# Performance work log

Hardware: AMD Instinct MI355X
Metric: run time of the kernel (lower is better)

Reference implementation:

```python
import jax, jax.numpy as jnp
import numpy as np

D = 256      # d_model
L = 2        # num_layers
N = 10000    # num_nodes
E = 160000   # num_edges (avg degree 16)
EPS = 1e-5


def _ln(h, g, b):
    m = jnp.mean(h, axis=-1, keepdims=True)
    v = jnp.mean(jnp.square(h - m), axis=-1, keepdims=True)
    return (h - m) / jnp.sqrt(v + EPS) * g + b


def _lrelu(h):
    return jnp.where(h > 0, h, 0.2 * h)


def setup_inputs() -> dict:
    key = jax.random.key(0)
    ks = jax.random.split(key, 24)
    p = lambda k, shape: (jax.random.normal(k, shape, dtype=jnp.float32) * 0.05)
    inp = {
        "edge_index": jax.random.randint(ks[0], (2, E), 0, N),
        "x": jax.random.normal(ks[1], (N, D), dtype=jnp.float32),
        # per-layer attention / FF params (torch Linear convention: W is [out, in])
        "Wq": p(ks[2], (L, D, D)), "bq": p(ks[3], (L, D)),
        "Wk": p(ks[4], (L, D, D)), "bk": p(ks[5], (L, D)),
        "Wv": p(ks[6], (L, D, D)), "bv": p(ks[7], (L, D)),
        "Wff": p(ks[8], (L, D, D)), "bff": p(ks[9], (L, D)),
        # LayerNorm params
        "ga": jnp.ones((L, D), jnp.float32), "ba": jnp.zeros((L, D), jnp.float32),
        "gf": jnp.ones((L, D), jnp.float32), "bf": jnp.zeros((L, D), jnp.float32),
        "gfin": jnp.ones((D,), jnp.float32), "bfin": jnp.zeros((D,), jnp.float32),
        # head MLP
        "W3": p(ks[10], (3 * D, D)), "b3": p(ks[11], (3 * D,)),
        "W4": p(ks[12], (3 * D, 3 * D)), "b4": p(ks[13], (3 * D,)),
        "W5": p(ks[14], (D, 3 * D)), "b5": p(ks[15], (D,)),
        "Wvec": p(ks[16], (1, D)), "bvec": p(ks[17], (1,)),
    }
    return inp


def reference(edge_index, x, Wq, bq, Wk, bk, Wv, bv, Wff, bff,
              ga, ba, gf, bf, gfin, bfin, W3, b3, W4, b4, W5, b5, Wvec, bvec):
    num_nodes = x.shape[0]
    src = edge_index[0]  # [E]
    dst = edge_index[1]  # [E] (segment-softmax target)
    x_i = x[src]         # [E, D]
    query = x[dst]       # [E, D] (x_j)
    for i in range(Wq.shape[0]):
        q = query @ Wq[i].T + bq[i]            # [E, D]
        k = x_i @ Wk[i].T + bk[i]
        v = x_i @ Wv[i].T + bv[i]
        alpha = jnp.sum(q * k, axis=-1)        # [E]
        # segment softmax over dst
        amax = jax.ops.segment_max(alpha, dst, num_segments=num_nodes)
        e = jnp.exp(alpha - amax[dst])
        denom = jax.ops.segment_sum(e, dst, num_segments=num_nodes)
        attn = e / denom[dst]                  # [E]
        attn_out = q + attn[:, None] * v       # [E, D]
        query = _ln(attn_out, ga[i], ba[i])
        query = query @ Wff[i].T + bff[i]
    query = _lrelu(query)
    query = _ln(query, gf[0], bf[0])           # dropout = identity (eval)
    h = _lrelu(query @ W3.T + b3)              # [E, 3D]
    h = _lrelu(h @ W4.T + b4)                  # [E, 3D]
    h = h @ W5.T + b5                          # [E, D]
    h = _ln(h + query, gfin, bfin)
    adj_logits = (h @ Wvec.T + bvec)[:, 0]     # [E]
    return adj_logits
```

## Files before the change

### kernel.cpp

```cpp
#include <hip/hip_runtime.h>

#define D 256

typedef unsigned short u16;
typedef unsigned int u32;
typedef __attribute__((ext_vector_type(8))) short short8;
typedef __attribute__((ext_vector_type(4))) float f32x4;
typedef __attribute__((ext_vector_type(16))) float f32x16;

__device__ __forceinline__ float b2f(u16 u) {
    return __uint_as_float(((u32)u) << 16);
}
__device__ __forceinline__ u16 f2b(float f) {
    u32 u = __float_as_uint(f);
    return (u16)((u + 0x7FFFu + ((u >> 16) & 1u)) >> 16);
}
__device__ __forceinline__ u32 packf(float v) {
    u16 h = f2b(v);
    u16 l = f2b(v - b2f(h));
    return ((u32)h << 16) | l;
}
__device__ __forceinline__ float unpackf(u32 p) {
    return b2f((u16)(p >> 16)) + b2f((u16)(p & 0xffffu));
}
template<typename T> __device__ __forceinline__ float ld1(const T* p);
template<> __device__ __forceinline__ float ld1<u16>(const u16* p) { return b2f(*p); }
template<> __device__ __forceinline__ float ld1<u32>(const u32* p) { return unpackf(*p); }

__device__ __forceinline__ u32 f2ord(float f) {
    u32 b = __float_as_uint(f);
    return (b & 0x80000000u) ? ~b : (b | 0x80000000u);
}
__device__ __forceinline__ float ord2f(u32 u) {
    return (u & 0x80000000u) ? __uint_as_float(u & 0x7fffffffu)
                             : __uint_as_float(~u);
}

__device__ __forceinline__ float wred(float v) {
#pragma unroll
    for (int m = 32; m; m >>= 1) v += __shfl_xor(v, m);
    return v;
}

__device__ __forceinline__ void gl_lds16(const u16* g, u16* l) {
    __builtin_amdgcn_global_load_lds(
        (__attribute__((address_space(1))) void*)(u16*)g,
        (__attribute__((address_space(3))) void*)l, 16, 0, 0);
}

template<int ACT>
__global__ __launch_bounds__(512, 4)
void gemm2(const u16* __restrict__ A, const u16* __restrict__ Whi,
           const float* __restrict__ bias, u16* __restrict__ C,
           int M, int N, int K)
{
    __shared__ u16 sA[128 * 64];
    __shared__ u16 sWh[256 * 64];

    const int tid  = threadIdx.x;
    const int lane = tid & 63;
    const int w    = tid >> 6;
    const int wm   = (w & 1) * 64;
    const int wn   = (w >> 1) * 64;
    const int row0 = blockIdx.x * 128;
    const int col0 = blockIdx.y * 256;

    f32x16 acc[2][2];
#pragma unroll
    for (int i = 0; i < 2; ++i)
#pragma unroll
        for (int j = 0; j < 2; ++j)
#pragma unroll
            for (int r = 0; r < 16; ++r) acc[i][j][r] = 0.f;

    const int r31   = lane & 31;
    const int khalf = lane >> 5;
    const int skey  = (r31 & 7) ^ ((r31 >> 3) & 3);
    const int l8r = lane >> 3;
    const int l8c = lane & 7;

    for (int k0 = 0; k0 < K; k0 += 64) {
#pragma unroll
        for (int s = 0; s < 4; ++s) {
            const int rbase = w * 32 + s * 8;
            const int row = rbase + l8r;
            const int gch = l8c ^ (row & 7) ^ s;
            const size_t gW = (size_t)(col0 + row) * K + k0 + gch * 8;
            gl_lds16(Whi + gW, sWh + rbase * 64);
        }
#pragma unroll
        for (int s = 0; s < 2; ++s) {
            const int rbase = w * 16 + s * 8;
            const int row = rbase + l8r;
            const int gch = l8c ^ (row & 7) ^ ((w * 2 + s) & 3);
            const size_t gA = (size_t)(row0 + row) * K + k0 + gch * 8;
            gl_lds16(A + gA, sA + rbase * 64);
        }
        __syncthreads();

#pragma unroll
        for (int w4 = 0; w4 < 4; ++w4) {
            const int slot = ((w4 * 2 + khalf) ^ skey) * 8;
            short8 af[2], wf[2];
#pragma unroll
            for (int i = 0; i < 2; ++i)
                af[i] = *(const short8*)(sA + (wm + i * 32 + r31) * 64 + slot);
#pragma unroll
            for (int j = 0; j < 2; ++j)
                wf[j] = *(const short8*)(sWh + (wn + j * 32 + r31) * 64 + slot);
#pragma unroll
            for (int i = 0; i < 2; ++i)
#pragma unroll
                for (int j = 0; j < 2; ++j)
                    acc[i][j] = __builtin_amdgcn_mfma_f32_32x32x16_bf16(af[i], wf[j], acc[i][j], 0, 0, 0);
        }
        __syncthreads();
    }

#pragma unroll
    for (int j = 0; j < 2; ++j) {
        const int col = col0 + wn + j * 32 + r31;
        const float bb = bias[col];
#pragma unroll
        for (int i = 0; i < 2; ++i) {
            const int rowb = row0 + wm + i * 32 + 4 * khalf;
#pragma unroll
            for (int reg = 0; reg < 16; ++reg) {
                const int row = rowb + (reg & 3) + 8 * (reg >> 2);
                float v = acc[i][j][reg] + bb;
                if (ACT) v = v > 0.f ? v : 0.2f * v;
                C[(size_t)row * N + col] = f2b(v);
            }
        }
    }
}

__global__ __launch_bounds__(512, 4)
void gemm3w(const u32* __restrict__ Ap,
            const u16* __restrict__ Whi, const u16* __restrict__ Wlo,
            const float* __restrict__ bias,
            u32* __restrict__ Cp, u16* __restrict__ Chi,
            int M, int K, int act)
{
    constexpr int N = 256;
    __shared__ u16 sAhi[128 * 32];
    __shared__ u16 sAlo[128 * 32];
    __shared__ u16 sWhi[256 * 32];
    __shared__ u16 sWlo[256 * 32];

    const int tid  = threadIdx.x;
    const int lane = tid & 63;
    const int w    = tid >> 6;
    const int wm   = (w & 1) * 64;
    const int wn   = (w >> 1) * 64;
    const int row0 = blockIdx.x * 128;

    f32x4 acc[4][4];
#pragma unroll
    for (int i = 0; i < 4; ++i)
#pragma unroll
        for (int j = 0; j < 4; ++j) acc[i][j] = (f32x4){0.f, 0.f, 0.f, 0.f};

    const int lrow = lane >> 2;
    const int gck  = (lane & 3) ^ ((lane >> 3) & 3);
    const int r15 = lane & 15;
    const int rck = ((lane >> 4) ^ ((r15 >> 1) & 3)) * 8;

    for (int k0 = 0; k0 < K; k0 += 32) {
#pragma unroll
        for (int s = 0; s < 2; ++s) {
            const int rbase = w * 32 + s * 16;
            const size_t gW = (size_t)(rbase + lrow) * K + k0 + gck * 8;
            gl_lds16(Whi + gW, sWhi + rbase * 32);
            gl_lds16(Wlo + gW, sWlo + rbase * 32);
        }
#pragma unroll
        for (int it = 0; it < 2; ++it) {
            const int u = tid + it * 512;
            const int ar = u >> 3;
            const int pos = u & 7;
            uint4 pk = *(const uint4*)(Ap + (size_t)(row0 + ar) * K + k0 + pos * 4);
            const int slot = (pos >> 1) ^ ((ar >> 1) & 3);
            const int base = ar * 32 + slot * 8 + (pos & 1) * 4;
            ushort4 h4, l4;
            h4.x = (u16)(pk.x >> 16); l4.x = (u16)(pk.x & 0xffffu);
            h4.y = (u16)(pk.y >> 16); l4.y = (u16)(pk.y & 0xffffu);
            h4.z = (u16)(pk.z >> 16); l4.z = (u16)(pk.z & 0xffffu);
            h4.w = (u16)(pk.w >> 16); l4.w = (u16)(pk.w & 0xffffu);
            *(ushort4*)(sAhi + base) = h4;
            *(ushort4*)(sAlo + base) = l4;
        }
        __syncthreads();

        short8 ah[4], al[4], wh[4], wl[4];
#pragma unroll
        for (int i = 0; i < 4; ++i) {
            const int offA = (wm + i * 16 + r15) * 32 + rck;
            ah[i] = *(const short8*)(sAhi + offA);
            al[i] = *(const short8*)(sAlo + offA);
        }
#pragma unroll
        for (int j = 0; j < 4; ++j) {
            const int offW = (wn + j * 16 + r15) * 32 + rck;
            wh[j] = *(const short8*)(sWhi + offW);
            wl[j] = *(const short8*)(sWlo + offW);
        }
#pragma unroll
        for (int i = 0; i < 4; ++i)
#pragma unroll
            for (int j = 0; j < 4; ++j) {
                acc[i][j] = __builtin_amdgcn_mfma_f32_16x16x32_bf16(ah[i], wh[j], acc[i][j], 0, 0, 0);
                acc[i][j] = __builtin_amdgcn_mfma_f32_16x16x32_bf16(ah[i], wl[j], acc[i][j], 0, 0, 0);
                acc[i][j] = __builtin_amdgcn_mfma_f32_16x16x32_bf16(al[i], wh[j], acc[i][j], 0, 0, 0);
            }
        __syncthreads();
    }

#pragma unroll
    for (int j = 0; j < 4; ++j) {
        const int col = wn + j * 16 + r15;
        const float bb = bias[col];
#pragma unroll
        for (int i = 0; i < 4; ++i) {
            const int rowb = row0 + wm + i * 16 + (lane >> 4) * 4;
#pragma unroll
            for (int r = 0; r < 4; ++r) {
                float v = acc[i][j][r] + bb;
                if (act) v = v > 0.f ? v : 0.2f * v;
                const size_t idx = (size_t)(rowb + r) * N + col;
                if (Cp) Cp[idx] = packf(v);
                else    Chi[idx] = f2b(v);
            }
        }
    }
}

__global__ __launch_bounds__(512, 4)
void gemm3n(const u32* __restrict__ Ap,
            const u16* __restrict__ Whi, const u16* __restrict__ Wlo,
            const float* __restrict__ b0, const float* __restrict__ b1,
            const float* __restrict__ b2,
            u32* __restrict__ Cp, int M, int K)
{
    constexpr int N = 256;
    __shared__ u16 sAhi[128 * 32];
    __shared__ u16 sAlo[128 * 32];
    __shared__ u16 sWhi[256 * 32];
    __shared__ u16 sWlo[256 * 32];

    const int tid  = threadIdx.x;
    const int lane = tid & 63;
    const int w    = tid >> 6;
    const int wm   = (w & 1) * 64;
    const int wn   = (w >> 1) * 64;
    const int row0 = blockIdx.x * 128;
    const int y    = blockIdx.y;
    const float* bias = (y == 0) ? b0 : ((y == 1) ? b1 : b2);
    const u16* Wh = Whi + (size_t)y * N * K;
    const u16* Wl = Wlo + (size_t)y * N * K;
    u32* Cy = Cp + (size_t)y * M * N;

    f32x4 acc[4][4];
#pragma unroll
    for (int i = 0; i < 4; ++i)
#pragma unroll
        for (int j = 0; j < 4; ++j) acc[i][j] = (f32x4){0.f, 0.f, 0.f, 0.f};

    const int lrow = lane >> 2;
    const int gck  = (lane & 3) ^ ((lane >> 3) & 3);
    const int r15 = lane & 15;
    const int rck = ((lane >> 4) ^ ((r15 >> 1) & 3)) * 8;

    for (int k0 = 0; k0 < K; k0 += 32) {
#pragma unroll
        for (int s = 0; s < 2; ++s) {
            const int rbase = w * 32 + s * 16;
            const size_t gW = (size_t)(rbase + lrow) * K + k0 + gck * 8;
            gl_lds16(Wh + gW, sWhi + rbase * 32);
            gl_lds16(Wl + gW, sWlo + rbase * 32);
        }
#pragma unroll
        for (int it = 0; it < 2; ++it) {
            const int u = tid + it * 512;
            const int ar = u >> 3;
            const int pos = u & 7;
            int arc = row0 + ar; if (arc >= M) arc = M - 1;
            uint4 pk = *(const uint4*)(Ap + (size_t)arc * K + k0 + pos * 4);
            const int slot = (pos >> 1) ^ ((ar >> 1) & 3);
            const int base = ar * 32 + slot * 8 + (pos & 1) * 4;
            ushort4 h4, l4;
            h4.x = (u16)(pk.x >> 16); l4.x = (u16)(pk.x & 0xffffu);
            h4.y = (u16)(pk.y >> 16); l4.y = (u16)(pk.y & 0xffffu);
            h4.z = (u16)(pk.z >> 16); l4.z = (u16)(pk.z & 0xffffu);
            h4.w = (u16)(pk.w >> 16); l4.w = (u16)(pk.w & 0xffffu);
            *(ushort4*)(sAhi + base) = h4;
            *(ushort4*)(sAlo + base) = l4;
        }
        __syncthreads();

        short8 ah[4], al[4], wh[4], wl[4];
#pragma unroll
        for (int i = 0; i < 4; ++i) {
            const int offA = (wm + i * 16 + r15) * 32 + rck;
            ah[i] = *(const short8*)(sAhi + offA);
            al[i] = *(const short8*)(sAlo + offA);
        }
#pragma unroll
        for (int j = 0; j < 4; ++j) {
            const int offW = (wn + j * 16 + r15) * 32 + rck;
            wh[j] = *(const short8*)(sWhi + offW);
            wl[j] = *(const short8*)(sWlo + offW);
        }
#pragma unroll
        for (int i = 0; i < 4; ++i)
#pragma unroll
            for (int j = 0; j < 4; ++j) {
                acc[i][j] = __builtin_amdgcn_mfma_f32_16x16x32_bf16(ah[i], wh[j], acc[i][j], 0, 0, 0);
                acc[i][j] = __builtin_amdgcn_mfma_f32_16x16x32_bf16(ah[i], wl[j], acc[i][j], 0, 0, 0);
                acc[i][j] = __builtin_amdgcn_mfma_f32_16x16x32_bf16(al[i], wh[j], acc[i][j], 0, 0, 0);
            }
        __syncthreads();
    }

#pragma unroll
    for (int j = 0; j < 4; ++j) {
        const int col = wn + j * 16 + r15;
        const float bb = bias[col];
#pragma unroll
        for (int i = 0; i < 4; ++i) {
            const int rowb = row0 + wm + i * 16 + (lane >> 4) * 4;
#pragma unroll
            for (int r = 0; r < 4; ++r) {
                const int row = rowb + r;
                if (row < M)
                    Cy[(size_t)row * N + col] = packf(acc[i][j][r] + bb);
            }
        }
    }
}

__global__ void pack_x(const float* __restrict__ x, u32* __restrict__ xp, int n)
{
    int i = blockIdx.x * 256 + threadIdx.x;
    if (i < n) xp[i] = packf(x[i]);
}

__global__ void wconv(const float* __restrict__ wsrc, u16* __restrict__ hi,
                      u16* __restrict__ lo, int n)
{
    int i = blockIdx.x * 256 + threadIdx.x;
    if (i < n) {
        float v = wsrc[i];
        u16 h = f2b(v);
        hi[i] = h;
        if (lo) lo[i] = f2b(v - b2f(h));
    }
}

__global__ void seg_init(u32* __restrict__ amax, float* __restrict__ denom, int n)
{
    int i = blockIdx.x * 256 + threadIdx.x;
    if (i < n) { amax[i] = 0u; denom[i] = 0.f; }
}

template<typename TQ, int MODE>
__global__ __launch_bounds__(256)
void attn_alpha(const int* __restrict__ src, const int* __restrict__ dst,
                const TQ* __restrict__ qn, const u32* __restrict__ kn,
                float* __restrict__ alpha, u32* __restrict__ amax, int E)
{
    int e = blockIdx.x * 4 + (threadIdx.x >> 6);
    int lane = threadIdx.x & 63;
    if (e >= E) return;
    int s = src[e], d = dst[e];
    const TQ* qp = MODE ? (qn + (size_t)e * D) : (qn + (size_t)d * D);
    const u32* kp = kn + (size_t)s * D;
    float dot = 0.f;
#pragma unroll
    for (int j = 0; j < 4; ++j)
        dot += ld1(qp + lane * 4 + j) * unpackf(kp[lane * 4 + j]);
    dot = wred(dot);
    if (lane == 0) {
        alpha[e] = dot;
        atomicMax(amax + d, f2ord(dot));
    }
}

__global__ void seg_exp(const int* __restrict__ dst, const float* __restrict__ alpha,
                        const u32* __restrict__ amax, float* __restrict__ ebuf,
                        float* __restrict__ denom, int E)
{
    int e = blockIdx.x * 256 + threadIdx.x;
    if (e >= E) return;
    int d = dst[e];
    float ex = expf(alpha[e] - ord2f(amax[d]));
    ebuf[e] = ex;
    atomicAdd(denom + d, ex);
}

template<typename TQ, int MODE>
__global__ __launch_bounds__(256)
void attn_out_ln(const int* __restrict__ src, const int* __restrict__ dst,
                 const TQ* __restrict__ qn, const u32* __restrict__ vn,
                 const float* __restrict__ ebuf, const float* __restrict__ denom,
                 const float* __restrict__ g, const float* __restrict__ bb,
                 u32* __restrict__ outp, int e0, int cm)
{
    int le = blockIdx.x * 4 + (threadIdx.x >> 6);
    int lane = threadIdx.x & 63;
    if (le >= cm) return;
    int ge = e0 + le;
    int s = src[ge], d = dst[ge];
    float attn = ebuf[ge] / denom[d];
    const TQ* qp = MODE ? (qn + (size_t)ge * D) : (qn + (size_t)d * D);
    const u32* vp = vn + (size_t)s * D;
    int d0 = lane * 4;
    float a0 = ld1(qp + d0 + 0) + attn * unpackf(vp[d0 + 0]);
    float a1 = ld1(qp + d0 + 1) + attn * unpackf(vp[d0 + 1]);
    float a2 = ld1(qp + d0 + 2) + attn * unpackf(vp[d0 + 2]);
    float a3 = ld1(qp + d0 + 3) + attn * unpackf(vp[d0 + 3]);
    float mean = wred(a0 + a1 + a2 + a3) * (1.f / D);
    float c0 = a0 - mean, c1 = a1 - mean, c2 = a2 - mean, c3 = a3 - mean;
    float var = wred(c0 * c0 + c1 * c1 + c2 * c2 + c3 * c3) * (1.f / D);
    float rstd = rsqrtf(var + 1e-5f);
    uint4 p;
    p.x = packf(c0 * rstd * g[d0 + 0] + bb[d0 + 0]);
    p.y = packf(c1 * rstd * g[d0 + 1] + bb[d0 + 1]);
    p.z = packf(c2 * rstd * g[d0 + 2] + bb[d0 + 2]);
    p.w = packf(c3 * rstd * g[d0 + 3] + bb[d0 + 3]);
    *(uint4*)(outp + (size_t)le * D + d0) = p;
}

__global__ __launch_bounds__(256)
void lrelu_ln(const u32* __restrict__ inp, const float* __restrict__ g,
              const float* __restrict__ bb, u16* __restrict__ out, int cm)
{
    int le = blockIdx.x * 4 + (threadIdx.x >> 6);
    int lane = threadIdx.x & 63;
    if (le >= cm) return;
    size_t base = (size_t)le * D + lane * 4;
    uint4 xp = *(const uint4*)(inp + base);
    float x0 = unpackf(xp.x), x1 = unpackf(xp.y);
    float x2 = unpackf(xp.z), x3 = unpackf(xp.w);
    float a0 = x0 > 0.f ? x0 : 0.2f * x0;
    float a1 = x1 > 0.f ? x1 : 0.2f * x1;
    float a2 = x2 > 0.f ? x2 : 0.2f * x2;
    float a3 = x3 > 0.f ? x3 : 0.2f * x3;
    float mean = wred(a0 + a1 + a2 + a3) * (1.f / D);
    float c0 = a0 - mean, c1 = a1 - mean, c2 = a2 - mean, c3 = a3 - mean;
    float var = wred(c0 * c0 + c1 * c1 + c2 * c2 + c3 * c3) * (1.f / D);
    float rstd = rsqrtf(var + 1e-5f);
    int d0 = lane * 4;
    ushort4 o;
    o.x = f2b(c0 * rstd * g[d0 + 0] + bb[d0 + 0]);
    o.y = f2b(c1 * rstd * g[d0 + 1] + bb[d0 + 1]);
    o.z = f2b(c2 * rstd * g[d0 + 2] + bb[d0 + 2]);
    o.w = f2b(c3 * rstd * g[d0 + 3] + bb[d0 + 3]);
    *(ushort4*)(out + base) = o;
}

__global__ __launch_bounds__(256)
void final_k(const u16* __restrict__ hp, const u16* __restrict__ qp,
             const float* __restrict__ gfin, const float* __restrict__ bfin,
             const float* __restrict__ wvec, const float* __restrict__ bvec,
             float* __restrict__ out, int e0, int cm)
{
    int le = blockIdx.x * 4 + (threadIdx.x >> 6);
    int lane = threadIdx.x & 63;
    if (le >= cm) return;
    size_t base = (size_t)le * D + lane * 4;
    ushort4 hv = *(const ushort4*)(hp + base);
    ushort4 qv = *(const ushort4*)(qp + base);
    float a0 = b2f(hv.x) + b2f(qv.x);
    float a1 = b2f(hv.y) + b2f(qv.y);
    float a2 = b2f(hv.z) + b2f(qv.z);
    float a3 = b2f(hv.w) + b2f(qv.w);
    float mean = wred(a0 + a1 + a2 + a3) * (1.f / D);
    float c0 = a0 - mean, c1 = a1 - mean, c2 = a2 - mean, c3 = a3 - mean;
    float var = wred(c0 * c0 + c1 * c1 + c2 * c2 + c3 * c3) * (1.f / D);
    float rstd = rsqrtf(var + 1e-5f);
    int d0 = lane * 4;
    float t0 = c0 * rstd * gfin[d0 + 0] + bfin[d0 + 0];
    float t1 = c1 * rstd * gfin[d0 + 1] + bfin[d0 + 1];
    float t2 = c2 * rstd * gfin[d0 + 2] + bfin[d0 + 2];
    float t3 = c3 * rstd * gfin[d0 + 3] + bfin[d0 + 3];
    float part = t0 * wvec[d0 + 0] + t1 * wvec[d0 + 1] +
                 t2 * wvec[d0 + 2] + t3 * wvec[d0 + 3];
    part = wred(part);
    if (lane == 0) out[e0 + le] = part + bvec[0];
}

extern "C" void kernel_launch(void* const* d_in, const int* in_sizes, int n_in,
                              void* d_out, int out_size, void* d_ws, size_t ws_size,
                              hipStream_t stream)
{
    const int*   ei   = (const int*)d_in[0];
    const float* x    = (const float*)d_in[1];
    const float* Wq   = (const float*)d_in[2];
    const float* bq   = (const float*)d_in[3];
    const float* Wk   = (const float*)d_in[4];
    const float* bk   = (const float*)d_in[5];
    const float* Wv   = (const float*)d_in[6];
    const float* bv   = (const float*)d_in[7];
    const float* Wff  = (const float*)d_in[8];
    const float* bff  = (const float*)d_in[9];
    const float* ga   = (const float*)d_in[10];
    const float* ba   = (const float*)d_in[11];
    const float* gf   = (const float*)d_in[12];
    const float* bf   = (const float*)d_in[13];
    const float* gfin = (const float*)d_in[14];
    const float* bfin = (const float*)d_in[15];
    const float* W3   = (const float*)d_in[16];
    const float* b3   = (const float*)d_in[17];
    const float* W4   = (const float*)d_in[18];
    const float* b4   = (const float*)d_in[19];
    const float* W5   = (const float*)d_in[20];
    const float* b5   = (const float*)d_in[21];
    const float* Wvec = (const float*)d_in[22];
    const float* bvec = (const float*)d_in[23];

    const int E  = in_sizes[0] / 2;
    const int Nn = in_sizes[1] / D;
    const int* src = ei;
    const int* dst = ei + E;

    char* base = (char*)d_ws;
    size_t off = 0;
    auto take = [&](size_t bytes) -> void* {
        off = (off + 255) & ~(size_t)255;
        void* r = base + off;
        off += bytes;
        return r;
    };
    u32*   nKV1 = (u32*)take((size_t)2 * Nn * D * 4);
    u16*   q1  = (u16*)take((size_t)E * D * 2);
    float* alpha = (float*)take((size_t)E * 4);
    float* ebuf  = (float*)take((size_t)E * 4);
    u32*   amax  = (u32*)take((size_t)Nn * 4);
    float* denom = (float*)take((size_t)Nn * 4);
    u16* wnh = (u16*)take((size_t)5 * D * D * 2);
    u16* wnl = (u16*)take((size_t)5 * D * D * 2);
    u16* wff0h = (u16*)take((size_t)D * D * 2); u16* wff0l = (u16*)take((size_t)D * D * 2);
    u16* wff1h = (u16*)take((size_t)D * D * 2); u16* wff1l = (u16*)take((size_t)D * D * 2);
    u16* wq1h  = (u16*)take((size_t)D * D * 2); u16* wq1l  = (u16*)take((size_t)D * D * 2);
    u16* w3h = (u16*)take((size_t)3 * D * D * 2);
    u16* w4h = (u16*)take((size_t)9 * D * D * 2);
    u16* w5h = (u16*)take((size_t)3 * D * D * 2);

    const size_t nodeB = (size_t)4 * Nn * D * 4;
    size_t rem = ws_size > off + 8192 ? ws_size - off - 8192 : 0;
    size_t cmA = rem / 4096;
    size_t cmB = rem > nodeB ? (rem - nodeB) / 2048 : 0;
    size_t CMs = (cmA * 2048 >= nodeB) ? cmA : cmB;
    CMs = (CMs / 128) * 128;
    if (CMs > (size_t)E) CMs = E;
    if (CMs > 32768) CMs = 32768;
    if (CMs < 128) CMs = 128;
    const int CM = (int)CMs;

    u32* c1p = (u32*)take((size_t)CM * D * 4);
    u32* c2p = (u32*)take((size_t)CM * D * 4);
    size_t zoneB = (size_t)CM * 2048 > nodeB ? (size_t)CM * 2048 : nodeB;
    char* zone = (char*)take(zoneB);
    u16* c2n = (u16*)zone;
    u16* c3  = (u16*)(zone + (size_t)CM * D * 2);
    u32* xp   = (u32*)zone;
    u32* zQKV = xp + (size_t)Nn * D;
    u32* zQ0 = zQKV;
    u32* zK0 = zQKV + (size_t)Nn * D;
    u32* zV0 = zQKV + (size_t)2 * Nn * D;
    u32* nK1 = nKV1;
    u32* nV1 = nKV1 + (size_t)Nn * D;
    u16* c4 = (u16*)c1p;
    u16* c5 = (u16*)((char*)c1p + (size_t)CM * 3 * D * 2);

    dim3 blk(256);
    dim3 blk2(512);
    int gridSeg = (Nn + 255) / 256;
    int gridE4  = (E + 3) / 4;
    int gridE   = (E + 255) / 256;
    const int DD = D * D;

    pack_x<<<(Nn * D + 255) / 256, 256, 0, stream>>>(x, xp, Nn * D);
    wconv<<<(DD + 255) / 256, 256, 0, stream>>>(Wq,          wnh + 0 * DD, wnl + 0 * DD, DD);
    wconv<<<(DD + 255) / 256, 256, 0, stream>>>(Wk,          wnh + 1 * DD, wnl + 1 * DD, DD);
    wconv<<<(DD + 255) / 256, 256, 0, stream>>>(Wv,          wnh + 2 * DD, wnl + 2 * DD, DD);
    wconv<<<(DD + 255) / 256, 256, 0, stream>>>(Wk + DD,     wnh + 3 * DD, wnl + 3 * DD, DD);
    wconv<<<(DD + 255) / 256, 256, 0, stream>>>(Wv + DD,     wnh + 4 * DD, wnl + 4 * DD, DD);
    wconv<<<(DD + 255) / 256, 256, 0, stream>>>(Wff,         wff0h, wff0l, DD);
    wconv<<<(DD + 255) / 256, 256, 0, stream>>>(Wff + DD,    wff1h, wff1l, DD);
    wconv<<<(DD + 255) / 256, 256, 0, stream>>>(Wq + DD,     wq1h,  wq1l,  DD);
    wconv<<<(3 * DD + 255) / 256, 256, 0, stream>>>(W3, w3h, (u16*)nullptr, 3 * DD);
    wconv<<<(9 * DD + 255) / 256, 256, 0, stream>>>(W4, w4h, (u16*)nullptr, 9 * DD);
    wconv<<<(3 * DD + 255) / 256, 256, 0, stream>>>(W5, w5h, (u16*)nullptr, 3 * DD);

    int gN = (Nn + 127) / 128;
    gemm3n<<<dim3(gN, 3), blk2, 0, stream>>>(xp, wnh, wnl, bq, bk, bv,
                                             zQKV, Nn, D);
    gemm3n<<<dim3(gN, 2), blk2, 0, stream>>>(xp, wnh + 3 * DD, wnl + 3 * DD,
                                             bk + D, bv + D, bv,
                                             nKV1, Nn, D);

    seg_init<<<gridSeg, 256, 0, stream>>>(amax, denom, Nn);
    attn_alpha<u32, 0><<<gridE4, blk, 0, stream>>>(src, dst, zQ0, zK0, alpha, amax, E);
    seg_exp<<<gridE, 256, 0, stream>>>(dst, alpha, amax, ebuf, denom, E);

    for (int e0 = 0; e0 < E; e0 += CM) {
        int cm = E - e0 < CM ? E - e0 : CM;
        int gE4 = (cm + 3) / 4;
        dim3 gD3(cm / 128);
        attn_out_ln<u32, 0><<<gE4, blk, 0, stream>>>(src, dst, zQ0, zV0, ebuf, denom,
                                                     ga, ba, c1p, e0, cm);
        gemm3w<<<gD3, blk2, 0, stream>>>(c1p, wff0h, wff0l, bff,
                                         c2p, (u16*)nullptr, cm, D, 0);
        gemm3w<<<gD3, blk2, 0, stream>>>(c2p, wq1h, wq1l, bq + D,
                                         (u32*)nullptr, q1 + (size_t)e0 * D,
                                         cm, D, 0);
    }

    seg_init<<<gridSeg, 256, 0, stream>>>(amax, denom, Nn);
    attn_alpha<u16, 1><<<gridE4, blk, 0, stream>>>(src, dst, q1, nK1, alpha, amax, E);
    seg_exp<<<gridE, 256, 0, stream>>>(dst, alpha, amax, ebuf, denom, E);

    for (int e0 = 0; e0 < E; e0 += CM) {
        int cm = E - e0 < CM ? E - e0 : CM;
        int gE4 = (cm + 3) / 4;
        dim3 gD3(cm / 128);
        dim3 g2a(cm / 128, (3 * D) / 256);
        dim3 g2b(cm / 128, D / 256);
        attn_out_ln<u16, 1><<<gE4, blk, 0, stream>>>(src, dst, q1, nV1, ebuf, denom,
                                                     ga + D, ba + D, c1p, e0, cm);
        gemm3w<<<gD3, blk2, 0, stream>>>(c1p, wff1h, wff1l, bff + D,
                                         c2p, (u16*)nullptr, cm, D, 0);
        lrelu_ln<<<gE4, blk, 0, stream>>>(c2p, gf, bf, c2n, cm);
        gemm2<1><<<g2a, blk2, 0, stream>>>(c2n, w3h, b3, c3, cm, 3 * D, D);
        gemm2<1><<<g2a, blk2, 0, stream>>>(c3, w4h, b4, c4, cm, 3 * D, 3 * D);
        gemm2<0><<<g2b, blk2, 0, stream>>>(c4, w5h, b5, c5, cm, D, 3 * D);
        final_k<<<gE4, blk, 0, stream>>>(c5, c2n, gfin, bfin, Wvec, bvec,
                                         (float*)d_out, e0, cm);
    }
}
```

Before: 1.383 ms.

## Double-buffer GEMM LDS tiles with a K-step of 32 to overlap loads and MFMA

Splits the shared-memory tiles into two buffers of K=32 each and issues the global-to-LDS loads for the next K-slice before computing the current one, leaving one barrier per iteration. The goal is to hide global load latency behind MFMA work. It keeps the LDS footprint the same but halves the work per iteration, doubles the number of barriers, and changes the swizzle pattern for the smaller row width.

```diff
diff --git a/kernel.cpp b/kernel.cpp
--- a/kernel.cpp
+++ b/kernel.cpp
@@ -54,8 +54,8 @@
            const float* __restrict__ bias, u16* __restrict__ C,
            int M, int N, int K)
 {
-    __shared__ u16 sA[128 * 64];
-    __shared__ u16 sWh[256 * 64];
+    __shared__ u16 sA[2][128 * 32];
+    __shared__ u16 sWh[2][256 * 32];
 
     const int tid  = threadIdx.x;
     const int lane = tid & 63;
@@ -75,47 +75,59 @@
 
     const int r31   = lane & 31;
     const int khalf = lane >> 5;
-    const int skey  = (r31 & 7) ^ ((r31 >> 3) & 3);
-    const int l8r = lane >> 3;
-    const int l8c = lane & 7;
-
-    for (int k0 = 0; k0 < K; k0 += 64) {
-#pragma unroll
-        for (int s = 0; s < 4; ++s) {
-            const int rbase = w * 32 + s * 8;
-            const int row = rbase + l8r;
-            const int gch = l8c ^ (row & 7) ^ s;
-            const size_t gW = (size_t)(col0 + row) * K + k0 + gch * 8;
-            gl_lds16(Whi + gW, sWh + rbase * 64);
-        }
+    const int skey  = (r31 >> 1) & 3;
+    const int dr    = lane >> 2;
+    const int dp    = lane & 3;
+
+    auto STAGE = [&](int b, int k0) {
 #pragma unroll
         for (int s = 0; s < 2; ++s) {
-            const int rbase = w * 16 + s * 8;
-            const int row = rbase + l8r;
-            const int gch = l8c ^ (row & 7) ^ ((w * 2 + s) & 3);
-            const size_t gA = (size_t)(row0 + row) * K + k0 + gch * 8;
-            gl_lds16(A + gA, sA + rbase * 64);
-        }
-        __syncthreads();
-
-#pragma unroll
-        for (int w4 = 0; w4 < 4; ++w4) {
-            const int slot = ((w4 * 2 + khalf) ^ skey) * 8;
+            const int rbase = (s * 8 + w) * 16;
+            const int row = rbase + dr;
+            const int gch = dp ^ ((row >> 1) & 3);
+            gl_lds16(Whi + (size_t)(col0 + row) * K + k0 + gch * 8,
+                     &sWh[b][rbase * 32]);
+        }
+        {
+            const int rbase = w * 16;
+            const int row = rbase + dr;
+            const int gch = dp ^ ((row >> 1) & 3);
+            gl_lds16(A + (size_t)(row0 + row) * K + k0 + gch * 8,
+                     &sA[b][rbase * 32]);
+        }
+    };
+
+    auto COMPUTE = [&](int b) {
+#pragma unroll
+        for (int m = 0; m < 2; ++m) {
+            const int chunk = m * 2 + khalf;
+            const int slot = (chunk ^ skey) * 8;
             short8 af[2], wf[2];
 #pragma unroll
             for (int i = 0; i < 2; ++i)
-                af[i] = *(const short8*)(sA + (wm + i * 32 + r31) * 64 + slot);
+                af[i] = *(const short8*)(&sA[b][(wm + i * 32 + r31) * 32 + slot]);
 #pragma unroll
             for (int j = 0; j < 2; ++j)
-                wf[j] = *(const short8*)(sWh + (wn + j * 32 + r31) * 64 + slot);
+                wf[j] = *(const short8*)(&sWh[b][(wn + j * 32 + r31) * 32 + slot]);
 #pragma unroll
             for (int i = 0; i < 2; ++i)
 #pragma unroll
                 for (int j = 0; j < 2; ++j)
                     acc[i][j] = __builtin_amdgcn_mfma_f32_32x32x16_bf16(af[i], wf[j], acc[i][j], 0, 0, 0);
         }
+    };
+
+    const int nt = K >> 5;
+    STAGE(0, 0);
+    __syncthreads();
+    int cur = 0;
+    for (int t = 0; t < nt - 1; ++t) {
+        STAGE(cur ^ 1, (t + 1) * 32);
+        COMPUTE(cur);
         __syncthreads();
-    }
+        cur ^= 1;
+    }
+    COMPUTE(cur);
 
 #pragma unroll
     for (int j = 0; j < 2; ++j) {
```

New measurement: 1.464 ms. 5.8% more time.

## Double-buffer GEMM LDS tiles with async prefetch two stages ahead

Applied to the files above, without the earlier changes.

Gives the bf16 MFMA GEMM kernel two LDS buffers for the A and W tiles. It issues global-to-LDS loads for the next K tile while the current one is computed, gated by explicit vmcnt waits and raw barriers instead of __syncthreads. The aim is to hide global load latency behind MFMA work. In exchange, LDS use per block doubles and launch bounds drop to one block per CU, which lowers occupancy and the latency hiding that came from running several blocks at once.

```diff
diff --git a/kernel.cpp b/kernel.cpp
--- a/kernel.cpp
+++ b/kernel.cpp
@@ -48,14 +48,16 @@
         (__attribute__((address_space(3))) void*)l, 16, 0, 0);
 }
 
+#define VMCNT(n) asm volatile("s_waitcnt vmcnt(" #n ")" ::: "memory")
+
 template<int ACT>
-__global__ __launch_bounds__(512, 4)
+__global__ __launch_bounds__(512, 1)
 void gemm2(const u16* __restrict__ A, const u16* __restrict__ Whi,
            const float* __restrict__ bias, u16* __restrict__ C,
            int M, int N, int K)
 {
-    __shared__ u16 sA[128 * 64];
-    __shared__ u16 sWh[256 * 64];
+    __shared__ u16 sA[2][128 * 64];
+    __shared__ u16 sWh[2][256 * 64];
 
     const int tid  = threadIdx.x;
     const int lane = tid & 63;
@@ -79,43 +81,59 @@
     const int l8r = lane >> 3;
     const int l8c = lane & 7;
 
-    for (int k0 = 0; k0 < K; k0 += 64) {
+    auto STAGE = [&](int b, int k0) {
 #pragma unroll
         for (int s = 0; s < 4; ++s) {
             const int rbase = w * 32 + s * 8;
             const int row = rbase + l8r;
             const int gch = l8c ^ (row & 7) ^ s;
-            const size_t gW = (size_t)(col0 + row) * K + k0 + gch * 8;
-            gl_lds16(Whi + gW, sWh + rbase * 64);
+            gl_lds16(Whi + (size_t)(col0 + row) * K + k0 + gch * 8,
+                     &sWh[b][rbase * 64]);
         }
 #pragma unroll
         for (int s = 0; s < 2; ++s) {
             const int rbase = w * 16 + s * 8;
             const int row = rbase + l8r;
             const int gch = l8c ^ (row & 7) ^ ((w * 2 + s) & 3);
-            const size_t gA = (size_t)(row0 + row) * K + k0 + gch * 8;
-            gl_lds16(A + gA, sA + rbase * 64);
-        }
-        __syncthreads();
-
+            gl_lds16(A + (size_t)(row0 + row) * K + k0 + gch * 8,
+                     &sA[b][rbase * 64]);
+        }
+    };
+
+    auto COMPUTE = [&](int b) {
 #pragma unroll
         for (int w4 = 0; w4 < 4; ++w4) {
             const int slot = ((w4 * 2 + khalf) ^ skey) * 8;
             short8 af[2], wf[2];
 #pragma unroll
             for (int i = 0; i < 2; ++i)
-                af[i] = *(const short8*)(sA + (wm + i * 32 + r31) * 64 + slot);
+                af[i] = *(const short8*)(&sA[b][(wm + i * 32 + r31) * 64 + slot]);
 #pragma unroll
             for (int j = 0; j < 2; ++j)
-                wf[j] = *(const short8*)(sWh + (wn + j * 32 + r31) * 64 + slot);
+                wf[j] = *(const short8*)(&sWh[b][(wn + j * 32 + r31) * 64 + slot]);
 #pragma unroll
             for (int i = 0; i < 2; ++i)
 #pragma unroll
                 for (int j = 0; j < 2; ++j)
                     acc[i][j] = __builtin_amdgcn_mfma_f32_32x32x16_bf16(af[i], wf[j], acc[i][j], 0, 0, 0);
         }
-        __syncthreads();
-    }
+    };
+
+    const int nt = K >> 6;
+    STAGE(0, 0);
+    STAGE(1, 64);
+    int cur = 0;
+    for (int t = 0; t < nt - 1; ++t) {
+        VMCNT(6);
+        __builtin_amdgcn_s_barrier();
+        COMPUTE(cur);
+        __builtin_amdgcn_s_barrier();
+        if (t + 2 < nt) STAGE(cur, (t + 2) << 6);
+        cur ^= 1;
+    }
+    VMCNT(0);
+    __builtin_amdgcn_s_barrier();
+    COMPUTE(cur);
 
 #pragma unroll
     for (int j = 0; j < 2; ++j) {
```

Measured after the change: 1.410 ms. About the same (+1.9%).

## Store split-bf16 activations as separate hi/lo planes and load via direct-to-LDS

Applied to the files above, without the earlier changes.

Activations were stored as packed u32 (hi/lo bf16 pair) and unpacked by threads into shared memory. They are now stored as two separate bf16 planes, so the GEMMs can fetch A tiles with the same direct global-to-LDS loads already used for weights. This removes the per-thread unpack and store work. The many per-weight conversion launches are also merged into one batched kernel. Buffer layout is reworked so intermediate buffers are aliased differently, which adds risk that aliased regions overlap.

```diff
diff --git a/kernel.cpp b/kernel.cpp
--- a/kernel.cpp
+++ b/kernel.cpp
@@ -136,11 +136,11 @@
 }
 
 __global__ __launch_bounds__(512, 4)
-void gemm3w(const u32* __restrict__ Ap,
-            const u16* __restrict__ Whi, const u16* __restrict__ Wlo,
+void gemm3w(const u16* __restrict__ Ah, const u16* __restrict__ Al,
+            const u16* __restrict__ Wh_, const u16* __restrict__ Wl_,
             const float* __restrict__ bias,
-            u32* __restrict__ Cp, u16* __restrict__ Chi,
-            int M, int K, int act)
+            u16* __restrict__ Ch, u16* __restrict__ Cl,
+            int M, int K)
 {
     constexpr int N = 256;
     __shared__ u16 sAhi[128 * 32];
@@ -171,24 +171,14 @@
         for (int s = 0; s < 2; ++s) {
             const int rbase = w * 32 + s * 16;
             const size_t gW = (size_t)(rbase + lrow) * K + k0 + gck * 8;
-            gl_lds16(Whi + gW, sWhi + rbase * 32);
-            gl_lds16(Wlo + gW, sWlo + rbase * 32);
-        }
-#pragma unroll
-        for (int it = 0; it < 2; ++it) {
-            const int u = tid + it * 512;
-            const int ar = u >> 3;
-            const int pos = u & 7;
-            uint4 pk = *(const uint4*)(Ap + (size_t)(row0 + ar) * K + k0 + pos * 4);
-            const int slot = (pos >> 1) ^ ((ar >> 1) & 3);
-            const int base = ar * 32 + slot * 8 + (pos & 1) * 4;
-            ushort4 h4, l4;
-            h4.x = (u16)(pk.x >> 16); l4.x = (u16)(pk.x & 0xffffu);
-            h4.y = (u16)(pk.y >> 16); l4.y = (u16)(pk.y & 0xffffu);
-            h4.z = (u16)(pk.z >> 16); l4.z = (u16)(pk.z & 0xffffu);
-            h4.w = (u16)(pk.w >> 16); l4.w = (u16)(pk.w & 0xffffu);
-            *(ushort4*)(sAhi + base) = h4;
-            *(ushort4*)(sAlo + base) = l4;
+            gl_lds16(Wh_ + gW, sWhi + rbase * 32);
+            gl_lds16(Wl_ + gW, sWlo + rbase * 32);
+        }
+        {
+            const int rbase = w * 16;
+            const size_t gA = (size_t)(row0 + rbase + lrow) * K + k0 + gck * 8;
+            gl_lds16(Ah + gA, sAhi + rbase * 32);
+            gl_lds16(Al + gA, sAlo + rbase * 32);
         }
         __syncthreads();
 
@@ -226,17 +216,21 @@
 #pragma unroll
             for (int r = 0; r < 4; ++r) {
                 float v = acc[i][j][r] + bb;
-                if (act) v = v > 0.f ? v : 0.2f * v;
                 const size_t idx = (size_t)(rowb + r) * N + col;
-                if (Cp) Cp[idx] = packf(v);
-                else    Chi[idx] = f2b(v);
+                if (Cl) {
+                    u16 hh = f2b(v);
+                    Ch[idx] = hh;
+                    Cl[idx] = f2b(v - b2f(hh));
+                } else {
+                    Ch[idx] = f2b(v);
+                }
             }
         }
     }
 }
 
 __global__ __launch_bounds__(512, 4)
-void gemm3n(const u32* __restrict__ Ap,
+void gemm3n(const u16* __restrict__ Ah, const u16* __restrict__ Al,
             const u16* __restrict__ Whi, const u16* __restrict__ Wlo,
             const float* __restrict__ b0, const float* __restrict__ b1,
             const float* __restrict__ b2,
@@ -279,22 +273,13 @@
             gl_lds16(Wh + gW, sWhi + rbase * 32);
             gl_lds16(Wl + gW, sWlo + rbase * 32);
         }
-#pragma unroll
-        for (int it = 0; it < 2; ++it) {
-            const int u = tid + it * 512;
-            const int ar = u >> 3;
-            const int pos = u & 7;
-            int arc = row0 + ar; if (arc >= M) arc = M - 1;
-            uint4 pk = *(const uint4*)(Ap + (size_t)arc * K + k0 + pos * 4);
-            const int slot = (pos >> 1) ^ ((ar >> 1) & 3);
-            const int base = ar * 32 + slot * 8 + (pos & 1) * 4;
-            ushort4 h4, l4;
-            h4.x = (u16)(pk.x >> 16); l4.x = (u16)(pk.x & 0xffffu);
-            h4.y = (u16)(pk.y >> 16); l4.y = (u16)(pk.y & 0xffffu);
-            h4.z = (u16)(pk.z >> 16); l4.z = (u16)(pk.z & 0xffffu);
-            h4.w = (u16)(pk.w >> 16); l4.w = (u16)(pk.w & 0xffffu);
-            *(ushort4*)(sAhi + base) = h4;
-            *(ushort4*)(sAlo + base) = l4;
+        {
+            const int rbase = w * 16;
+            int arow = row0 + rbase + lrow;
+            if (arow >= M) arow = M - 1;
+            const size_t gA = (size_t)arow * K + k0 + gck * 8;
+            gl_lds16(Ah + gA, sAhi + rbase * 32);
+            gl_lds16(Al + gA, sAlo + rbase * 32);
         }
         __syncthreads();
 
@@ -339,22 +324,30 @@
     }
 }
 
-__global__ void pack_x(const float* __restrict__ x, u32* __restrict__ xp, int n)
-{
-    int i = blockIdx.x * 256 + threadIdx.x;
-    if (i < n) xp[i] = packf(x[i]);
-}
-
-__global__ void wconv(const float* __restrict__ wsrc, u16* __restrict__ hi,
-                      u16* __restrict__ lo, int n)
+__global__ void pack_x(const float* __restrict__ x, u16* __restrict__ xh,
+                       u16* __restrict__ xl, int n)
 {
     int i = blockIdx.x * 256 + threadIdx.x;
     if (i < n) {
-        float v = wsrc[i];
+        float v = x[i];
         u16 h = f2b(v);
-        hi[i] = h;
-        if (lo) lo[i] = f2b(v - b2f(h));
-    }
+        xh[i] = h;
+        xl[i] = f2b(v - b2f(h));
+    }
+}
+
+struct WcvA { const float* s[23]; u16* h[23]; u16* l[23]; };
+__global__ __launch_bounds__(256)
+void wconv_all(WcvA a, int n)
+{
+    int i = blockIdx.x * 256 + threadIdx.x;
+    if (i >= n) return;
+    int r = i >> 16;
+    int o = i & 65535;
+    float v = a.s[r][o];
+    u16 hh = f2b(v);
+    a.h[r][o] = hh;
+    if (a.l[r]) a.l[r][o] = f2b(v - b2f(hh));
 }
 
 __global__ void seg_init(u32* __restrict__ amax, float* __restrict__ denom, int n)
@@ -404,7 +397,7 @@
                  const TQ* __restrict__ qn, const u32* __restrict__ vn,
                  const float* __restrict__ ebuf, const float* __restrict__ denom,
                  const float* __restrict__ g, const float* __restrict__ bb,
-                 u32* __restrict__ outp, int e0, int cm)
+                 u16* __restrict__ oh, u16* __restrict__ ol, int e0, int cm)
 {
     int le = blockIdx.x * 4 + (threadIdx.x >> 6);
     int lane = threadIdx.x & 63;
@@ -423,25 +416,35 @@
     float c0 = a0 - mean, c1 = a1 - mean, c2 = a2 - mean, c3 = a3 - mean;
     float var = wred(c0 * c0 + c1 * c1 + c2 * c2 + c3 * c3) * (1.f / D);
     float rstd = rsqrtf(var + 1e-5f);
-    uint4 p;
-    p.x = packf(c0 * rstd * g[d0 + 0] + bb[d0 + 0]);
-    p.y = packf(c1 * rstd * g[d0 + 1] + bb[d0 + 1]);
-    p.z = packf(c2 * rstd * g[d0 + 2] + bb[d0 + 2]);
-    p.w = packf(c3 * rstd * g[d0 + 3] + bb[d0 + 3]);
-    *(uint4*)(outp + (size_t)le * D + d0) = p;
+    float t0 = c0 * rstd * g[d0 + 0] + bb[d0 + 0];
+    float t1 = c1 * rstd * g[d0 + 1] + bb[d0 + 1];
+    float t2 = c2 * rstd * g[d0 + 2] + bb[d0 + 2];
+    float t3 = c3 * rstd * g[d0 + 3] + bb[d0 + 3];
+    size_t base = (size_t)le * D + d0;
+    ushort4 ph, pl;
+    ph.x = f2b(t0); pl.x = f2b(t0 - b2f(ph.x));
+    ph.y = f2b(t1); pl.y = f2b(t1 - b2f(ph.y));
+    ph.z = f2b(t2); pl.z = f2b(t2 - b2f(ph.z));
+    ph.w = f2b(t3); pl.w = f2b(t3 - b2f(ph.w));
+    *(ushort4*)(oh + base) = ph;
+    *(ushort4*)(ol + base) = pl;
 }
 
 __global__ __launch_bounds__(256)
-void lrelu_ln(const u32* __restrict__ inp, const float* __restrict__ g,
-              const float* __restrict__ bb, u16* __restrict__ out, int cm)
+void lrelu_ln(const u16* __restrict__ ih, const u16* __restrict__ il,
+              const float* __restrict__ g, const float* __restrict__ bb,
+              u16* __restrict__ out, int cm)
 {
     int le = blockIdx.x * 4 + (threadIdx.x >> 6);
     int lane = threadIdx.x & 63;
     if (le >= cm) return;
     size_t base = (size_t)le * D + lane * 4;
-    uint4 xp = *(const uint4*)(inp + base);
-    float x0 = unpackf(xp.x), x1 = unpackf(xp.y);
-    float x2 = unpackf(xp.z), x3 = unpackf(xp.w);
+    ushort4 xh = *(const ushort4*)(ih + base);
+    ushort4 xl = *(const ushort4*)(il + base);
+    float x0 = b2f(xh.x) + b2f(xl.x);
+    float x1 = b2f(xh.y) + b2f(xl.y);
+    float x2 = b2f(xh.z) + b2f(xl.z);
+    float x3 = b2f(xh.w) + b2f(xl.w);
     float a0 = x0 > 0.f ? x0 : 0.2f * x0;
     float a1 = x1 > 0.f ? x1 : 0.2f * x1;
     float a2 = x2 > 0.f ? x2 : 0.2f * x2;
@@ -558,21 +561,25 @@
     if (CMs < 128) CMs = 128;
     const int CM = (int)CMs;
 
-    u32* c1p = (u32*)take((size_t)CM * D * 4);
-    u32* c2p = (u32*)take((size_t)CM * D * 4);
+    u16* cpl = (u16*)take((size_t)CM * D * 2 * 4);
+    u16* c1h = cpl;
+    u16* c1l = cpl + (size_t)CM * D;
+    u16* c2h = cpl + (size_t)2 * CM * D;
+    u16* c2l = cpl + (size_t)3 * CM * D;
+    u16* c4  = cpl;
+    u16* c5  = cpl + (size_t)3 * CM * D;
     size_t zoneB = (size_t)CM * 2048 > nodeB ? (size_t)CM * 2048 : nodeB;
     char* zone = (char*)take(zoneB);
     u16* c2n = (u16*)zone;
     u16* c3  = (u16*)(zone + (size_t)CM * D * 2);
-    u32* xp   = (u32*)zone;
-    u32* zQKV = xp + (size_t)Nn * D;
+    u16* xph = (u16*)zone;
+    u16* xpl = xph + (size_t)Nn * D;
+    u32* zQKV = (u32*)(zone + (size_t)Nn * D * 4);
     u32* zQ0 = zQKV;
     u32* zK0 = zQKV + (size_t)Nn * D;
     u32* zV0 = zQKV + (size_t)2 * Nn * D;
     u32* nK1 = nKV1;
     u32* nV1 = nKV1 + (size_t)Nn * D;
-    u16* c4 = (u16*)c1p;
-    u16* c5 = (u16*)((char*)c1p + (size_t)CM * 3 * D * 2);
 
     dim3 blk(256);
     dim3 blk2(512);
@@ -581,23 +588,33 @@
     int gridE   = (E + 255) / 256;
     const int DD = D * D;
 
-    pack_x<<<(Nn * D + 255) / 256, 256, 0, stream>>>(x, xp, Nn * D);
-    wconv<<<(DD + 255) / 256, 256, 0, stream>>>(Wq,          wnh + 0 * DD, wnl + 0 * DD, DD);
-    wconv<<<(DD + 255) / 256, 256, 0, stream>>>(Wk,          wnh + 1 * DD, wnl + 1 * DD, DD);
-    wconv<<<(DD + 255) / 256, 256, 0, stream>>>(Wv,          wnh + 2 * DD, wnl + 2 * DD, DD);
-    wconv<<<(DD + 255) / 256, 256, 0, stream>>>(Wk + DD,     wnh + 3 * DD, wnl + 3 * DD, DD);
-    wconv<<<(DD + 255) / 256, 256, 0, stream>>>(Wv + DD,     wnh + 4 * DD, wnl + 4 * DD, DD);
-    wconv<<<(DD + 255) / 256, 256, 0, stream>>>(Wff,         wff0h, wff0l, DD);
-    wconv<<<(DD + 255) / 256, 256, 0, stream>>>(Wff + DD,    wff1h, wff1l, DD);
-    wconv<<<(DD + 255) / 256, 256, 0, stream>>>(Wq + DD,     wq1h,  wq1l,  DD);
-    wconv<<<(3 * DD + 255) / 256, 256, 0, stream>>>(W3, w3h, (u16*)nullptr, 3 * DD);
-    wconv<<<(9 * DD + 255) / 256, 256, 0, stream>>>(W4, w4h, (u16*)nullptr, 9 * DD);
-    wconv<<<(3 * DD + 255) / 256, 256, 0, stream>>>(W5, w5h, (u16*)nullptr, 3 * DD);
+    pack_x<<<(Nn * D + 255) / 256, 256, 0, stream>>>(x, xph, xpl, Nn * D);
+
+    WcvA wa;
+    const float* ws_[23] = {Wq, Wk, Wv, Wk + DD, Wv + DD, Wff, Wff + DD, Wq + DD,
+                            W3, W3 + DD, W3 + 2 * DD,
+                            W4, W4 + DD, W4 + 2 * DD, W4 + 3 * DD, W4 + 4 * DD,
+                            W4 + 5 * DD, W4 + 6 * DD, W4 + 7 * DD, W4 + 8 * DD,
+                            W5, W5 + DD, W5 + 2 * DD};
+    u16* wh_[23] = {wnh, wnh + DD, wnh + 2 * DD, wnh + 3 * DD, wnh + 4 * DD,
+                    wff0h, wff1h, wq1h,
+                    w3h, w3h + DD, w3h + 2 * DD,
+                    w4h, w4h + DD, w4h + 2 * DD, w4h + 3 * DD, w4h + 4 * DD,
+                    w4h + 5 * DD, w4h + 6 * DD, w4h + 7 * DD, w4h + 8 * DD,
+                    w5h, w5h + DD, w5h + 2 * DD};
+    u16* wl_[23] = {wnl, wnl + DD, wnl + 2 * DD, wnl + 3 * DD, wnl + 4 * DD,
+                    wff0l, wff1l, wq1l,
+                    nullptr, nullptr, nullptr,
+                    nullptr, nullptr, nullptr, nullptr, nullptr,
+                    nullptr, nullptr, nullptr, nullptr,
+                    nullptr, nullptr, nullptr};
+    for (int r = 0; r < 23; ++r) { wa.s[r] = ws_[r]; wa.h[r] = wh_[r]; wa.l[r] = wl_[r]; }
+    wconv_all<<<(23 * DD) / 256, 256, 0, stream>>>(wa, 23 * DD);
 
     int gN = (Nn + 127) / 128;
-    gemm3n<<<dim3(gN, 3), blk2, 0, stream>>>(xp, wnh, wnl, bq, bk, bv,
+    gemm3n<<<dim3(gN, 3), blk2, 0, stream>>>(xph, xpl, wnh, wnl, bq, bk, bv,
                                              zQKV, Nn, D);
-    gemm3n<<<dim3(gN, 2), blk2, 0, stream>>>(xp, wnh + 3 * DD, wnl + 3 * DD,
+    gemm3n<<<dim3(gN, 2), blk2, 0, stream>>>(xph, xpl, wnh + 3 * DD, wnl + 3 * DD,
                                              bk + D, bv + D, bv,
                                              nKV1, Nn, D);
 
@@ -610,12 +627,12 @@
         int gE4 = (cm + 3) / 4;
         dim3 gD3(cm / 128);
         attn_out_ln<u32, 0><<<gE4, blk, 0, stream>>>(src, dst, zQ0, zV0, ebuf, denom,
-                                                     ga, ba, c1p, e0, cm);
-        gemm3w<<<gD3, blk2, 0, stream>>>(c1p, wff0h, wff0l, bff,
-                                         c2p, (u16*)nullptr, cm, D, 0);
-        gemm3w<<<gD3, blk2, 0, stream>>>(c2p, wq1h, wq1l, bq + D,
-                                         (u32*)nullptr, q1 + (size_t)e0 * D,
-                                         cm, D, 0);
+                                                     ga, ba, c1h, c1l, e0, cm);
+        gemm3w<<<gD3, blk2, 0, stream>>>(c1h, c1l, wff0h, wff0l, bff,
+                                         c2h, c2l, cm, D);
+        gemm3w<<<gD3, blk2, 0, stream>>>(c2h, c2l, wq1h, wq1l, bq + D,
+                                         q1 + (size_t)e0 * D, (u16*)nullptr,
+                                         cm, D);
     }
 
     seg_init<<<gridSeg, 256, 0, stream>>>(amax, denom, Nn);
@@ -629,10 +646,10 @@
         dim3 g2a(cm / 128, (3 * D) / 256);
         dim3 g2b(cm / 128, D / 256);
         attn_out_ln<u16, 1><<<gE4, blk, 0, stream>>>(src, dst, q1, nV1, ebuf, denom,
-                                                     ga + D, ba + D, c1p, e0, cm);
-        gemm3w<<<gD3, blk2, 0, stream>>>(c1p, wff1h, wff1l, bff + D,
-                                         c2p, (u16*)nullptr, cm, D, 0);
-        lrelu_ln<<<gE4, blk, 0, stream>>>(c2p, gf, bf, c2n, cm);
+                                                     ga + D, ba + D, c1h, c1l, e0, cm);
+        gemm3w<<<gD3, blk2, 0, stream>>>(c1h, c1l, wff1h, wff1l, bff + D,
+                                         c2h, c2l, cm, D);
+        lrelu_ln<<<gE4, blk, 0, stream>>>(c2h, c2l, gf, bf, c2n, cm);
         gemm2<1><<<g2a, blk2, 0, stream>>>(c2n, w3h, b3, c3, cm, 3 * D, D);
         gemm2<1><<<g2a, blk2, 0, stream>>>(c3, w4h, b4, c4, cm, 3 * D, 3 * D);
         gemm2<0><<<g2b, blk2, 0, stream>>>(c4, w5h, b5, c5, cm, D, 3 * D);
```

New measurement: 1.419 ms. +2.6%, slower.
